# Kernel optimization log

Measured on AMD Instinct MI355X. Metric: run time of the kernel, lower is better.

The kernel has to match this reference:

```python
import jax, jax.numpy as jnp
import numpy as np


def haar_level(x):
    """One 2D Haar (periodization-equivalent for even sizes) DWT on [B,K,C,H,W].
    Returns [B,4K,C,H/2,W/2] with per-parent band order (LL, Hx, Hy, Hxy),
    matching the tree's append order yl, yh0, yh1, yh2."""
    B, K, C, H, W = x.shape
    x = x.reshape(B, K, C, H // 2, 2, W // 2, 2)
    a = x[:, :, :, :, 0, :, 0]
    b = x[:, :, :, :, 0, :, 1]
    c = x[:, :, :, :, 1, :, 0]
    d = x[:, :, :, :, 1, :, 1]
    ll = (a + b + c + d) * 0.5
    h1 = (a - b + c - d) * 0.5   # high along width
    h2 = (a + b - c - d) * 0.5   # high along height
    h3 = (a - b - c + d) * 0.5   # diagonal
    out = jnp.stack([ll, h1, h2, h3], axis=2)  # [B,K,4,C,H/2,W/2]
    return out.reshape(B, 4 * K, C, H // 2, W // 2)


def conv2d(x, w, b, stride, pad):
    y = jax.lax.conv_general_dilated(
        x, w, window_strides=(stride, stride),
        padding=[(pad, pad), (pad, pad)],
        dimension_numbers=('NCHW', 'OIHW', 'NCHW'))
    return y + b[None, :, None, None]


def setup_inputs() -> dict:
    key = jax.random.key(0)
    ks = jax.random.split(key, 9)
    s = 0.05
    return {
        'x':        jax.random.normal(ks[0], (64, 3, 224, 224), dtype=jnp.float32),
        'w_s1':     jax.random.normal(ks[1], (192, 3, 7, 7), dtype=jnp.float32) * s,
        'b_s1':     jax.random.normal(ks[2], (192,), dtype=jnp.float32) * s,
        'w_s2':     jax.random.normal(ks[3], (192, 192, 7, 7), dtype=jnp.float32) * s,
        'b_s2':     jax.random.normal(ks[4], (192,), dtype=jnp.float32) * s,
        'w_p':      jax.random.normal(ks[5], (768, 960, 3, 3), dtype=jnp.float32) * s,
        'b_p':      jax.random.normal(ks[6], (768,), dtype=jnp.float32) * s,
        'cls_token': jax.random.normal(ks[7], (1, 1, 768), dtype=jnp.float32),
        'positions': jax.random.normal(ks[8], (50, 768), dtype=jnp.float32),
    }


def reference(x, w_s1, b_s1, w_s2, b_s2, w_p, b_p, cls_token, positions):
    B = x.shape[0]
    # ---- 4-level full Haar wavelet packet tree (vectorized over subbands) ----
    t = x[:, None]                      # [B,1,3,224,224]
    for _ in range(4):
        t = haar_level(t)               # -> [B,256,3,14,14]
    wav = t.reshape(B, 256 * 3, 14, 14)  # [B,768,14,14] (tree concat order)
    # ---- spatial branch: two strided 7x7 convs (224 -> 56 -> 14) ----
    sp = conv2d(x, w_s1, b_s1, stride=4, pad=3)
    sp = conv2d(sp, w_s2, b_s2, stride=4, pad=3)   # [B,192,14,14]
    feat = jnp.concatenate([wav, sp], axis=1)      # [B,960,14,14]
    # ---- patch projection conv 3x3 s2 -> 7x7, flatten to tokens ----
    y = conv2d(feat, w_p, b_p, stride=2, pad=1)    # [B,768,7,7]
    y = y.reshape(B, 768, 49).transpose(0, 2, 1)   # [B,49,768]
    cls = jnp.broadcast_to(cls_token, (B, 1, 768))
    y = jnp.concatenate([cls, y], axis=1) + positions  # [B,50,768]
    return y
```

## Files before the change

kernel.cpp:

```cpp
#include <hip/hip_runtime.h>
#include <stdint.h>

typedef __attribute__((ext_vector_type(8))) short short8;
typedef __attribute__((ext_vector_type(4))) float floatx4;

__device__ inline unsigned short f2bf(float f){
  union { float fv; unsigned int u; } v; v.fv = f;
  unsigned int u = v.u;
  unsigned int r = ((u >> 16) & 1u) + 0x7FFFu;
  return (unsigned short)((u + r) >> 16);
}

__device__ __forceinline__ void async16(const void* g, void* l){
  __builtin_amdgcn_global_load_lds(
      (const __attribute__((address_space(1))) unsigned int*)g,
      (__attribute__((address_space(3))) unsigned int*)l, 16, 0, 0);
}

__global__ void prep_w1(const float* __restrict__ w, unsigned short* __restrict__ w1p){
  int i = blockIdx.x*256 + threadIdx.x;
  if (i >= 192*192) return;
  int k = i % 192, o = i / 192;
  int cc = k >> 3, kx = k & 7;
  unsigned short v = 0;
  if (cc < 21 && kx < 7){
    int c = cc / 7, ky = cc % 7;
    v = f2bf(w[(o*3 + c)*49 + ky*7 + kx]);
  }
  w1p[i] = v;
}
__global__ void prep_w2(const float* __restrict__ w, unsigned short* __restrict__ w2p){
  int i = blockIdx.x*256 + threadIdx.x;
  if (i >= 192*9408) return;
  int k = i % 9408, o = i / 9408;
  int g = k / 192, c = k % 192;
  int ky = g / 7, kx = g % 7;
  w2p[i] = f2bf(w[((o*192 + c)*7 + ky)*7 + kx]);
}
__global__ void prep_w3(const float* __restrict__ w, unsigned short* __restrict__ w3p){
  int i = blockIdx.x*256 + threadIdx.x;
  if (i >= 768*8640) return;
  int k = i % 8640, o = i / 8640;
  int g = k / 960, c = k % 960;
  int ky = g / 3, kx = g % 3;
  w3p[i] = f2bf(w[((o*960 + c)*3 + ky)*3 + kx]);
}
__global__ void prep_zp(unsigned int* __restrict__ zp){
  zp[threadIdx.x] = 0u;
}

__global__ void pad_x2(const float* __restrict__ x, unsigned short* __restrict__ xh2){
  int idx = blockIdx.x*256 + threadIdx.x;
  if (idx >= 64*3*230*56*8) return;
  int kx = idx & 7; int t = idx >> 3;
  int ox = t % 56;  t /= 56;
  int iy = t % 230; t /= 230;
  int row = iy - 3;
  int col = 4*ox - 3 + kx;
  unsigned short v = 0;
  if (row >= 0 && row < 224 && col >= 0 && col < 224)
    v = f2bf(x[((size_t)t*224 + row)*224 + col]);
  xh2[idx] = v;
}

__global__ void wavelet_kernel(const float* __restrict__ x, unsigned short* __restrict__ feat){
  int blk = blockIdx.x;
  int j = blk % 14; blk /= 14;
  int i = blk % 14; blk /= 14;
  int c = blk % 3;  int b = blk / 3;
  int t = threadIdx.x;
  int u = t >> 4, v = t & 15;
  float val = x[((size_t)(b*3 + c)*224 + (i*16 + u))*224 + (j*16 + v)];
  #pragma unroll
  for (int bit = 1; bit < 64; bit <<= 1){
    float p = __shfl_xor(val, bit);
    val = (t & bit) ? (p - val) : (val + p);
  }
  __shared__ float s[256];
  #pragma unroll
  for (int bit = 64; bit < 256; bit <<= 1){
    s[t] = val; __syncthreads();
    float p = s[t ^ bit]; __syncthreads();
    val = (t & bit) ? (p - val) : (val + p);
  }
  s[t] = val; __syncthreads();
  int k = t;
  int d1 = (k>>6)&3, d2 = (k>>4)&3, d3 = (k>>2)&3, d4 = k&3;
  int mr = (d1>>1) | ((d2>>1)<<1) | ((d3>>1)<<2) | ((d4>>1)<<3);
  int mc = (d1&1)  | ((d2&1)<<1)  | ((d3&1)<<2)  | ((d4&1)<<3);
  float outv = s[mr*16 + mc] * 0.0625f;
  feat[((size_t)((b*14 + i)*14 + j))*960 + (k*3 + c)] = f2bf(outv);
}

__global__ __launch_bounds__(256) void conv1_gemm(const unsigned short* __restrict__ xh2,
                                                  const unsigned short* __restrict__ w1p,
                                                  const float* __restrict__ b1,
                                                  unsigned short* __restrict__ sp1){
  __shared__ unsigned short As[2][128*64], Bs[2][64*64];
  int m0 = blockIdx.x*128, n0 = blockIdx.y*64;
  int tid = threadIdx.x, wave = tid >> 6, lane = tid & 63;
  int l16 = lane & 15, quad = lane >> 4;
  int wy = wave >> 1, wx = wave & 1;
  int r8 = lane >> 3, kb = (lane & 7) ^ r8;

  int Abase[4];
  #pragma unroll
  for (int j = 0; j < 4; j++){
    int row = wave*32 + j*8 + r8;
    int m = m0 + row;
    int ox = m % 56; int t = m / 56; int oy = t % 56; int b = t / 56;
    Abase[j] = (b*690 + 4*oy)*448 + ox*8;
  }
  const unsigned short* pB0 = w1p + (n0 + wave*16 + r8)*192 + kb*8;
  const unsigned short* pB1 = pB0 + 8*192;

  int sw = l16 & 7;
  int xo0 = ((quad    ) ^ sw)*8;
  int xo1 = ((quad + 4) ^ sw)*8;
  int aoff[4];
  #pragma unroll
  for (int mt = 0; mt < 4; mt++) aoff[mt] = (wy*64 + mt*16 + l16)*64;
  int boff0 = (wx*32 + l16)*64, boff1 = boff0 + 16*64;

  floatx4 acc[4][2];
  #pragma unroll
  for (int mt = 0; mt < 4; mt++)
    #pragma unroll
    for (int nt = 0; nt < 2; nt++) acc[mt][nt] = (floatx4){0.f,0.f,0.f,0.f};

  auto stage = [&](int i, int buf){
    int cc = i*8 + kb;
    int c = (cc*147) >> 10;
    int ky = cc - 7*c;
    int koff = (c*230 + ky)*448;
    #pragma unroll
    for (int j = 0; j < 4; j++)
      async16(xh2 + Abase[j] + koff, (void*)&As[buf][(wave*32 + j*8)*64]);
    async16(pB0 + i*64, (void*)&Bs[buf][(wave*16    )*64]);
    async16(pB1 + i*64, (void*)&Bs[buf][(wave*16 + 8)*64]);
  };

  stage(0, 0);
  __syncthreads();
  #pragma unroll
  for (int i = 0; i < 3; i++){
    int buf = i & 1;
    if (i < 2) stage(i+1, buf ^ 1);
    #pragma unroll
    for (int ks = 0; ks < 2; ks++){
      int xo = ks ? xo1 : xo0;
      short8 b0 = *(const short8*)&Bs[buf][boff0 + xo];
      short8 b1 = *(const short8*)&Bs[buf][boff1 + xo];
      #pragma unroll
      for (int mt = 0; mt < 4; mt++){
        short8 a = *(const short8*)&As[buf][aoff[mt] + xo];
        acc[mt][0] = __builtin_amdgcn_mfma_f32_16x16x32_bf16(a, b0, acc[mt][0], 0, 0, 0);
        acc[mt][1] = __builtin_amdgcn_mfma_f32_16x16x32_bf16(a, b1, acc[mt][1], 0, 0, 0);
      }
    }
    __syncthreads();
  }

  #pragma unroll
  for (int mt = 0; mt < 4; mt++){
    #pragma unroll
    for (int rg = 0; rg < 4; rg++){
      int row = wy*64 + mt*16 + quad*4 + rg;
      size_t ob = (size_t)(m0 + row)*192;
      #pragma unroll
      for (int nt = 0; nt < 2; nt++){
        int nn = n0 + wx*32 + nt*16 + l16;
        sp1[ob + nn] = f2bf(acc[mt][nt][rg] + b1[nn]);
      }
    }
  }
}

template<int MODE>
__global__ __launch_bounds__(256) void conv_gemm(const unsigned short* __restrict__ Ain,
                                                 const unsigned short* __restrict__ Bt,
                                                 const float* __restrict__ bias,
                                                 const float* __restrict__ pos,
                                                 const unsigned short* __restrict__ zp,
                                                 void* __restrict__ outp){
  constexpr int OH  = (MODE==2) ? 14 : 7;
  constexpr int OW  = OH;
  constexpr int IH  = (MODE==2) ? 56 : 14;
  constexpr int IW  = IH;
  constexpr int Cin = (MODE==2) ? 192 : 960;
  constexpr int KW  = (MODE==2) ? 7 : 3;
  constexpr int S   = (MODE==2) ? 4 : 2;
  constexpr int P   = (MODE==2) ? 3 : 1;
  constexpr int K   = (MODE==2) ? 9408 : 8640;
  constexpr int NIT = K/64;
  constexpr int MTI = (MODE==2) ? 196 : 49;
  constexpr int GRP = (MODE==2) ? 24 : 96;

  int id = blockIdx.x;
  int g = id / GRP, rem = id % GRP;
  int mtile = g*8 + (rem & 7), ntile = rem >> 3;
  if (mtile >= MTI) return;
  int m0 = mtile*64, n0 = ntile*64;

  __shared__ unsigned short As[2][64*64], Bs[2][64*64];
  int tid = threadIdx.x, wave = tid >> 6, lane = tid & 63;
  int l16 = lane & 15, quad = lane >> 4;
  int wy = wave >> 1, wx = wave & 1;

  int r8 = lane >> 3, kb = (lane & 7) ^ r8;
  int rA0 = wave*16 + r8, rA1 = rA0 + 8;

  int m_0 = m0 + rA0;
  int ox0 = m_0 % OW; int t0 = m_0 / OW; int oy0 = t0 % OH; int bb0 = t0 / OH;
  int iyb0 = S*oy0 - P, ixb0 = S*ox0 - P;
  int abase0 = ((bb0*IH + iyb0)*IW + ixb0)*Cin + kb*8;
  int m_1 = m0 + rA1;
  int ox1 = m_1 % OW; int t1 = m_1 / OW; int oy1 = t1 % OH; int bb1 = t1 / OH;
  int iyb1 = S*oy1 - P, ixb1 = S*ox1 - P;
  int abase1 = ((bb1*IH + iyb1)*IW + ixb1)*Cin + kb*8;

  const unsigned short* pB0 = Bt + (size_t)(n0 + rA0)*K + kb*8;
  const unsigned short* pB1 = Bt + (size_t)(n0 + rA1)*K + kb*8;

  int sw = l16 & 7;
  int xo0 = ((quad    ) ^ sw)*8;
  int xo1 = ((quad + 4) ^ sw)*8;
  int aoff0 = (wy*32      + l16)*64;
  int aoff1 = (wy*32 + 16 + l16)*64;
  int boff0 = (wx*32      + l16)*64;
  int boff1 = (wx*32 + 16 + l16)*64;

  floatx4 acc[2][2];
  #pragma unroll
  for (int a = 0; a < 2; a++)
    #pragma unroll
    for (int bq = 0; bq < 2; bq++) acc[a][bq] = (floatx4){0.f,0.f,0.f,0.f};

  int c0 = 0, ky = 0, kx = 0, k0n = 0;

  auto stage = [&](int buf){
    int koff = (ky*IW + kx)*Cin + c0;
    int iy0 = iyb0 + ky, ix0 = ixb0 + kx;
    int iy1 = iyb1 + ky, ix1 = ixb1 + kx;
    const unsigned short* pa0 = ((unsigned)iy0 < (unsigned)IH && (unsigned)ix0 < (unsigned)IW)
                                ? (Ain + (abase0 + koff)) : zp;
    const unsigned short* pa1 = ((unsigned)iy1 < (unsigned)IH && (unsigned)ix1 < (unsigned)IW)
                                ? (Ain + (abase1 + koff)) : zp;
    async16(pa0, (void*)&As[buf][(wave*16    )*64]);
    async16(pa1, (void*)&As[buf][(wave*16 + 8)*64]);
    async16(pB0 + k0n, (void*)&Bs[buf][(wave*16    )*64]);
    async16(pB1 + k0n, (void*)&Bs[buf][(wave*16 + 8)*64]);
    k0n += 64;
    c0 += 64;
    if (c0 == Cin){ c0 = 0; kx++; if (kx == KW){ kx = 0; ky++; } }
  };

  stage(0);
  __syncthreads();
  for (int i = 0; i < NIT; i++){
    int buf = i & 1;
    if (i + 1 < NIT) stage(buf ^ 1);
    #pragma unroll
    for (int ks = 0; ks < 2; ks++){
      int xo = ks ? xo1 : xo0;
      short8 a0 = *(const short8*)&As[buf][aoff0 + xo];
      short8 a1 = *(const short8*)&As[buf][aoff1 + xo];
      short8 b0 = *(const short8*)&Bs[buf][boff0 + xo];
      short8 b1 = *(const short8*)&Bs[buf][boff1 + xo];
      acc[0][0] = __builtin_amdgcn_mfma_f32_16x16x32_bf16(a0, b0, acc[0][0], 0, 0, 0);
      acc[0][1] = __builtin_amdgcn_mfma_f32_16x16x32_bf16(a0, b1, acc[0][1], 0, 0, 0);
      acc[1][0] = __builtin_amdgcn_mfma_f32_16x16x32_bf16(a1, b0, acc[1][0], 0, 0, 0);
      acc[1][1] = __builtin_amdgcn_mfma_f32_16x16x32_bf16(a1, b1, acc[1][1], 0, 0, 0);
    }
    __syncthreads();
  }

  #pragma unroll
  for (int mt = 0; mt < 2; mt++){
    #pragma unroll
    for (int rg = 0; rg < 4; rg++){
      int row = wy*32 + mt*16 + quad*4 + rg;
      int mm = m0 + row;
      #pragma unroll
      for (int nt = 0; nt < 2; nt++){
        int nn = n0 + wx*32 + nt*16 + l16;
        float v = acc[mt][nt][rg] + bias[nn];
        if (MODE == 2){
          ((unsigned short*)outp)[(size_t)mm*960 + 768 + nn] = f2bf(v);
        } else {
          int b2 = mm / 49;
          int tt = mm - b2*49;
          v += pos[(size_t)(1 + tt)*768 + nn];
          ((float*)outp)[((size_t)(mm + b2 + 1))*768 + nn] = v;
        }
      }
    }
  }
}

__global__ void cls_kernel(const float* __restrict__ cls, const float* __restrict__ pos,
                           float* __restrict__ out){
  int i = blockIdx.x*256 + threadIdx.x;
  if (i >= 64*768) return;
  int e = i % 768, b = i / 768;
  out[(size_t)(b*50)*768 + e] = cls[e] + pos[e];
}

extern "C" void kernel_launch(void* const* d_in, const int* in_sizes, int n_in,
                              void* d_out, int out_size, void* d_ws, size_t ws_size,
                              hipStream_t stream){
  (void)in_sizes; (void)n_in; (void)out_size;
  const float* x    = (const float*)d_in[0];
  const float* w_s1 = (const float*)d_in[1];
  const float* b_s1 = (const float*)d_in[2];
  const float* w_s2 = (const float*)d_in[3];
  const float* b_s2 = (const float*)d_in[4];
  const float* w_p  = (const float*)d_in[5];
  const float* b_p  = (const float*)d_in[6];
  const float* cls  = (const float*)d_in[7];
  const float* pos  = (const float*)d_in[8];
  float* out = (float*)d_out;

  char* ws = (char*)d_ws;
  if (ws_size < 118235136u) return;
  unsigned short* w1p  = (unsigned short*)(ws + 0);
  unsigned short* sp1  = (unsigned short*)(ws + 131072);
  unsigned short* zp   = (unsigned short*)(ws + 77201408u);
  unsigned short* w2p  = (unsigned short*)(ws + 77266944u);
  unsigned short* w3p  = (unsigned short*)(ws + 80879616u);
  unsigned short* feat = (unsigned short*)(ws + 94150656u);
  unsigned short* xh2  = (unsigned short*)(ws + 77266944u);

  prep_w1<<<(192*192 + 255)/256, 256, 0, stream>>>(w_s1, w1p);
  pad_x2<<<(64*3*230*56*8)/256, 256, 0, stream>>>(x, xh2);
  conv1_gemm<<<dim3(1568, 3), 256, 0, stream>>>(xh2, w1p, b_s1, sp1);
  prep_w2<<<(192*9408 + 255)/256, 256, 0, stream>>>(w_s2, w2p);
  prep_w3<<<(768*8640 + 255)/256, 256, 0, stream>>>(w_p, w3p);
  prep_zp<<<1, 64, 0, stream>>>((unsigned int*)zp);
  wavelet_kernel<<<64*3*14*14, 256, 0, stream>>>(x, feat);
  conv_gemm<2><<<600, 256, 0, stream>>>(sp1, w2p, b_s2, nullptr, zp, (void*)feat);
  conv_gemm<3><<<672, 256, 0, stream>>>(feat, w3p, b_p, pos, zp, (void*)out);
  cls_kernel<<<(64*768 + 255)/256, 256, 0, stream>>>(cls, pos, out);
}
```

Before: 434.6 us.

## Split K across waves in conv GEMMs with deeper async pipeline and LDS reduction

Each wave now computes the full 64x64 output tile over its own K-slice (split-K within the block), using BK=128 stages with two buffers in flight and fine-grained vmcnt barriers. Partial accumulators are reduced through LDS and written with vectorized stores. The weight K dimension is padded to a multiple of 128 with zeros, and out-of-range A taps go to the zero page. This aims to cut LDS reads per MFMA and barrier overhead, at the cost of more accumulator registers and an extra reduction pass.

Measured after the change: 528.7 us. 1.22x slower.

```diff
diff --git a/kernel.cpp b/kernel.cpp
--- a/kernel.cpp
+++ b/kernel.cpp
@@ -16,6 +16,18 @@
       (const __attribute__((address_space(1))) unsigned int*)g,
       (__attribute__((address_space(3))) unsigned int*)l, 16, 0, 0);
 }
+
+#define PBAR(N) do {                                               \
+    asm volatile("s_waitcnt vmcnt(" #N ")" ::: "memory");          \
+    __builtin_amdgcn_s_barrier();                                  \
+    asm volatile("" ::: "memory");                                 \
+  } while (0)
+
+#define LBAR do {                                                  \
+    asm volatile("s_waitcnt lgkmcnt(0)" ::: "memory");             \
+    __builtin_amdgcn_s_barrier();                                  \
+    asm volatile("" ::: "memory");                                 \
+  } while (0)
 
 __global__ void prep_w1(const float* __restrict__ w, unsigned short* __restrict__ w1p){
   int i = blockIdx.x*256 + threadIdx.x;
@@ -31,19 +43,27 @@
 }
 __global__ void prep_w2(const float* __restrict__ w, unsigned short* __restrict__ w2p){
   int i = blockIdx.x*256 + threadIdx.x;
-  if (i >= 192*9408) return;
-  int k = i % 9408, o = i / 9408;
-  int g = k / 192, c = k % 192;
-  int ky = g / 7, kx = g % 7;
-  w2p[i] = f2bf(w[((o*192 + c)*7 + ky)*7 + kx]);
+  if (i >= 192*9472) return;
+  int k = i % 9472, o = i / 9472;
+  unsigned short v = 0;
+  if (k < 9408){
+    int g = k / 192, c = k % 192;
+    int ky = g / 7, kx = g % 7;
+    v = f2bf(w[((o*192 + c)*7 + ky)*7 + kx]);
+  }
+  w2p[i] = v;
 }
 __global__ void prep_w3(const float* __restrict__ w, unsigned short* __restrict__ w3p){
   int i = blockIdx.x*256 + threadIdx.x;
-  if (i >= 768*8640) return;
-  int k = i % 8640, o = i / 8640;
-  int g = k / 960, c = k % 960;
-  int ky = g / 3, kx = g % 3;
-  w3p[i] = f2bf(w[((o*960 + c)*3 + ky)*3 + kx]);
+  if (i >= 768*8704) return;
+  int k = i % 8704, o = i / 8704;
+  unsigned short v = 0;
+  if (k < 8640){
+    int g = k / 960, c = k % 960;
+    int ky = g / 3, kx = g % 3;
+    v = f2bf(w[((o*960 + c)*3 + ky)*3 + kx]);
+  }
+  w3p[i] = v;
 }
 __global__ void prep_zp(unsigned int* __restrict__ zp){
   zp[threadIdx.x] = 0u;
@@ -191,8 +211,8 @@
   constexpr int KW  = (MODE==2) ? 7 : 3;
   constexpr int S   = (MODE==2) ? 4 : 2;
   constexpr int P   = (MODE==2) ? 3 : 1;
-  constexpr int K   = (MODE==2) ? 9408 : 8640;
-  constexpr int NIT = K/64;
+  constexpr int KP  = (MODE==2) ? 9472 : 8704;
+  constexpr int NIT = KP/128;
   constexpr int MTI = (MODE==2) ? 196 : 49;
   constexpr int GRP = (MODE==2) ? 24 : 96;
 
@@ -202,98 +222,118 @@
   if (mtile >= MTI) return;
   int m0 = mtile*64, n0 = ntile*64;
 
-  __shared__ unsigned short As[2][64*64], Bs[2][64*64];
-  int tid = threadIdx.x, wave = tid >> 6, lane = tid & 63;
+  __shared__ __align__(16) unsigned short As[2][8192];
+  __shared__ __align__(16) unsigned short Bs[2][8192];
+  int tid = threadIdx.x, w = tid >> 6, lane = tid & 63;
   int l16 = lane & 15, quad = lane >> 4;
-  int wy = wave >> 1, wx = wave & 1;
-
-  int r8 = lane >> 3, kb = (lane & 7) ^ r8;
-  int rA0 = wave*16 + r8, rA1 = rA0 + 8;
-
-  int m_0 = m0 + rA0;
-  int ox0 = m_0 % OW; int t0 = m_0 / OW; int oy0 = t0 % OH; int bb0 = t0 / OH;
-  int iyb0 = S*oy0 - P, ixb0 = S*ox0 - P;
-  int abase0 = ((bb0*IH + iyb0)*IW + ixb0)*Cin + kb*8;
-  int m_1 = m0 + rA1;
-  int ox1 = m_1 % OW; int t1 = m_1 / OW; int oy1 = t1 % OH; int bb1 = t1 / OH;
-  int iyb1 = S*oy1 - P, ixb1 = S*ox1 - P;
-  int abase1 = ((bb1*IH + iyb1)*IW + ixb1)*Cin + kb*8;
-
-  const unsigned short* pB0 = Bt + (size_t)(n0 + rA0)*K + kb*8;
-  const unsigned short* pB1 = Bt + (size_t)(n0 + rA1)*K + kb*8;
-
-  int sw = l16 & 7;
-  int xo0 = ((quad    ) ^ sw)*8;
-  int xo1 = ((quad + 4) ^ sw)*8;
-  int aoff0 = (wy*32      + l16)*64;
-  int aoff1 = (wy*32 + 16 + l16)*64;
-  int boff0 = (wx*32      + l16)*64;
-  int boff1 = (wx*32 + 16 + l16)*64;
-
-  floatx4 acc[2][2];
-  #pragma unroll
-  for (int a = 0; a < 2; a++)
-    #pragma unroll
-    for (int bq = 0; bq < 2; bq++) acc[a][bq] = (floatx4){0.f,0.f,0.f,0.f};
-
-  int c0 = 0, ky = 0, kx = 0, k0n = 0;
+
+  int Abase[4], iybj[4], ixbj[4], cj[4], kyj[4], kxj[4];
+  const unsigned short* Bp[4];
+  #pragma unroll
+  for (int j = 0; j < 4; j++){
+    int r  = w*16 + j*4 + quad;
+    int gc = l16 ^ (r & 15);
+    int m = m0 + r;
+    int ox = m % OW; int t = m / OW; int oy = t % OH; int bb = t / OH;
+    iybj[j] = S*oy - P; ixbj[j] = S*ox - P;
+    Abase[j] = ((bb*IH + iybj[j])*IW + ixbj[j])*Cin;
+    cj[j] = gc*8; kyj[j] = 0; kxj[j] = 0;
+    Bp[j] = Bt + (size_t)(n0 + r)*KP + gc*8;
+  }
 
   auto stage = [&](int buf){
-    int koff = (ky*IW + kx)*Cin + c0;
-    int iy0 = iyb0 + ky, ix0 = ixb0 + kx;
-    int iy1 = iyb1 + ky, ix1 = ixb1 + kx;
-    const unsigned short* pa0 = ((unsigned)iy0 < (unsigned)IH && (unsigned)ix0 < (unsigned)IW)
-                                ? (Ain + (abase0 + koff)) : zp;
-    const unsigned short* pa1 = ((unsigned)iy1 < (unsigned)IH && (unsigned)ix1 < (unsigned)IW)
-                                ? (Ain + (abase1 + koff)) : zp;
-    async16(pa0, (void*)&As[buf][(wave*16    )*64]);
-    async16(pa1, (void*)&As[buf][(wave*16 + 8)*64]);
-    async16(pB0 + k0n, (void*)&Bs[buf][(wave*16    )*64]);
-    async16(pB1 + k0n, (void*)&Bs[buf][(wave*16 + 8)*64]);
-    k0n += 64;
-    c0 += 64;
-    if (c0 == Cin){ c0 = 0; kx++; if (kx == KW){ kx = 0; ky++; } }
+    #pragma unroll
+    for (int j = 0; j < 4; j++){
+      int iy = iybj[j] + kyj[j], ix = ixbj[j] + kxj[j];
+      bool ok = ((unsigned)iy < (unsigned)IH) && ((unsigned)ix < (unsigned)IW) && (kyj[j] < KW);
+      const unsigned short* pa = ok
+          ? (Ain + Abase[j] + (kyj[j]*IW + kxj[j])*Cin + cj[j]) : zp;
+      async16(pa, (void*)&As[buf][(w*16 + j*4)*128]);
+    }
+    #pragma unroll
+    for (int j = 0; j < 4; j++){
+      async16(Bp[j], (void*)&Bs[buf][(w*16 + j*4)*128]);
+      Bp[j] += 128;
+    }
+    #pragma unroll
+    for (int j = 0; j < 4; j++){
+      cj[j] += 128;
+      if (cj[j] >= Cin){ cj[j] -= Cin; kxj[j]++; if (kxj[j] == KW){ kxj[j] = 0; kyj[j]++; } }
+    }
   };
 
-  stage(0);
+  int ch = ((w*4 + quad) ^ l16) * 8;
+  int aoff[4], boff[4];
+  #pragma unroll
+  for (int mt = 0; mt < 4; mt++) aoff[mt] = (mt*16 + l16)*128 + ch;
+  #pragma unroll
+  for (int nt = 0; nt < 4; nt++) boff[nt] = (nt*16 + l16)*128 + ch;
+
+  floatx4 acc[4][4];
+  #pragma unroll
+  for (int mt = 0; mt < 4; mt++)
+    #pragma unroll
+    for (int nt = 0; nt < 4; nt++) acc[mt][nt] = (floatx4){0.f,0.f,0.f,0.f};
+
+  auto compute = [&](int buf){
+    short8 af[4], bf[4];
+    #pragma unroll
+    for (int mt = 0; mt < 4; mt++) af[mt] = *(const short8*)&As[buf][aoff[mt]];
+    #pragma unroll
+    for (int nt = 0; nt < 4; nt++) bf[nt] = *(const short8*)&Bs[buf][boff[nt]];
+    #pragma unroll
+    for (int mt = 0; mt < 4; mt++)
+      #pragma unroll
+      for (int nt = 0; nt < 4; nt++)
+        acc[mt][nt] = __builtin_amdgcn_mfma_f32_16x16x32_bf16(af[mt], bf[nt], acc[mt][nt], 0, 0, 0);
+  };
+
+  stage(0); stage(1);
+  for (int i = 0; i < NIT - 2; i++){
+    PBAR(8);
+    compute(i & 1);
+    LBAR;
+    stage(i & 1);
+  }
+  PBAR(8); compute(NIT & 1);
+  PBAR(0); compute((NIT - 1) & 1);
   __syncthreads();
-  for (int i = 0; i < NIT; i++){
-    int buf = i & 1;
-    if (i + 1 < NIT) stage(buf ^ 1);
-    #pragma unroll
-    for (int ks = 0; ks < 2; ks++){
-      int xo = ks ? xo1 : xo0;
-      short8 a0 = *(const short8*)&As[buf][aoff0 + xo];
-      short8 a1 = *(const short8*)&As[buf][aoff1 + xo];
-      short8 b0 = *(const short8*)&Bs[buf][boff0 + xo];
-      short8 b1 = *(const short8*)&Bs[buf][boff1 + xo];
-      acc[0][0] = __builtin_amdgcn_mfma_f32_16x16x32_bf16(a0, b0, acc[0][0], 0, 0, 0);
-      acc[0][1] = __builtin_amdgcn_mfma_f32_16x16x32_bf16(a0, b1, acc[0][1], 0, 0, 0);
-      acc[1][0] = __builtin_amdgcn_mfma_f32_16x16x32_bf16(a1, b0, acc[1][0], 0, 0, 0);
-      acc[1][1] = __builtin_amdgcn_mfma_f32_16x16x32_bf16(a1, b1, acc[1][1], 0, 0, 0);
-    }
-    __syncthreads();
-  }
-
-  #pragma unroll
-  for (int mt = 0; mt < 2; mt++){
-    #pragma unroll
-    for (int rg = 0; rg < 4; rg++){
-      int row = wy*32 + mt*16 + quad*4 + rg;
-      int mm = m0 + row;
+
+  float* red = (w < 2) ? ((float*)As + (w << 12)) : ((float*)Bs + ((w - 2) << 12));
+  #pragma unroll
+  for (int mt = 0; mt < 4; mt++)
+    #pragma unroll
+    for (int nt = 0; nt < 4; nt++)
       #pragma unroll
-      for (int nt = 0; nt < 2; nt++){
-        int nn = n0 + wx*32 + nt*16 + l16;
-        float v = acc[mt][nt][rg] + bias[nn];
-        if (MODE == 2){
-          ((unsigned short*)outp)[(size_t)mm*960 + 768 + nn] = f2bf(v);
-        } else {
-          int b2 = mm / 49;
-          int tt = mm - b2*49;
-          v += pos[(size_t)(1 + tt)*768 + nn];
-          ((float*)outp)[((size_t)(mm + b2 + 1))*768 + nn] = v;
-        }
-      }
+      for (int rg = 0; rg < 4; rg++)
+        red[(mt*16 + quad*4 + rg)*64 + nt*16 + l16] = acc[mt][nt][rg];
+  __syncthreads();
+
+  float* r0 = (float*)As;
+  float* r1 = (float*)As + 4096;
+  float* r2 = (float*)Bs;
+  float* r3 = (float*)Bs + 4096;
+  #pragma unroll
+  for (int rp = 0; rp < 4; rp++){
+    int row = w*16 + rp*4 + quad;
+    int off = row*64 + l16*4;
+    floatx4 s = *(floatx4*)&r0[off];
+    s += *(floatx4*)&r1[off];
+    s += *(floatx4*)&r2[off];
+    s += *(floatx4*)&r3[off];
+    int nn = n0 + l16*4;
+    s += *(const floatx4*)&bias[nn];
+    int mm = m0 + row;
+    if (MODE == 2){
+      uint2 pk;
+      pk.x = (unsigned)f2bf(s[0]) | ((unsigned)f2bf(s[1]) << 16);
+      pk.y = (unsigned)f2bf(s[2]) | ((unsigned)f2bf(s[3]) << 16);
+      *(uint2*)&((unsigned short*)outp)[(size_t)mm*960 + 768 + nn] = pk;
+    } else {
+      int b2 = mm / 49;
+      int tt = mm - b2*49;
+      s += *(const floatx4*)&pos[(size_t)(1 + tt)*768 + nn];
+      *(floatx4*)&((float*)outp)[((size_t)(mm + b2 + 1))*768 + nn] = s;
     }
   }
 }
@@ -322,20 +362,20 @@
   float* out = (float*)d_out;
 
   char* ws = (char*)d_ws;
-  if (ws_size < 118235136u) return;
+  if (ws_size < 118358016u) return;
   unsigned short* w1p  = (unsigned short*)(ws + 0);
   unsigned short* sp1  = (unsigned short*)(ws + 131072);
   unsigned short* zp   = (unsigned short*)(ws + 77201408u);
   unsigned short* w2p  = (unsigned short*)(ws + 77266944u);
-  unsigned short* w3p  = (unsigned short*)(ws + 80879616u);
-  unsigned short* feat = (unsigned short*)(ws + 94150656u);
+  unsigned short* w3p  = (unsigned short*)(ws + 80904192u);
+  unsigned short* feat = (unsigned short*)(ws + 94273536u);
   unsigned short* xh2  = (unsigned short*)(ws + 77266944u);
 
   prep_w1<<<(192*192 + 255)/256, 256, 0, stream>>>(w_s1, w1p);
   pad_x2<<<(64*3*230*56*8)/256, 256, 0, stream>>>(x, xh2);
   conv1_gemm<<<dim3(1568, 3), 256, 0, stream>>>(xh2, w1p, b_s1, sp1);
-  prep_w2<<<(192*9408 + 255)/256, 256, 0, stream>>>(w_s2, w2p);
-  prep_w3<<<(768*8640 + 255)/256, 256, 0, stream>>>(w_p, w3p);
+  prep_w2<<<(192*9472 + 255)/256, 256, 0, stream>>>(w_s2, w2p);
+  prep_w3<<<(768*8704 + 255)/256, 256, 0, stream>>>(w_p, w3p);
   prep_zp<<<1, 64, 0, stream>>>((unsigned int*)zp);
   wavelet_kernel<<<64*3*14*14, 256, 0, stream>>>(x, feat);
   conv_gemm<2><<<600, 256, 0, stream>>>(sp1, w2p, b_s2, nullptr, zp, (void*)feat);
```
